# Optimization experiments

Measured on AMD Instinct MI355X. Metric: run time of the kernel, lower is better.

## Reference

```python
import jax, jax.numpy as jnp
import numpy as np

CK, CV, CS = 8, 120, 64          # key / value / spatial-basis channels
NUM_AGENTS, NQ_PER = 4, 4        # queries chunked per agent; chunk(a,4) hard-codes NQ_PER=4
HID = 256                        # lstm_hidden_size
NA = 18                          # num_actions
U = 8                            # Fourier freqs; CS = U*U = 64
MLP_W = 512                      # q/a mlp hidden width


def spatial_basis(h, w):
    # fixed (h, w, CS) cos-product Fourier basis (SpatialBasis buffer)
    ph = jnp.arange(1, h + 1, dtype=jnp.float32)[:, None] * jnp.ones((1, w), jnp.float32) * (np.pi / h)
    pw = jnp.ones((h, 1), jnp.float32) * jnp.arange(1, w + 1, dtype=jnp.float32)[None, :] * (np.pi / w)
    u = jnp.arange(1, U + 1, dtype=jnp.float32)
    ca = jnp.cos(ph[..., None] * u)   # (h, w, U)
    cb = jnp.cos(pw[..., None] * u)   # (h, w, U)
    return jnp.einsum('hwu,hwv->hwuv', ca, cb).reshape(h, w, U * U)


def mlp3(x, w0, b0, w1, b1, w2, b2):
    # build_mlp with 2 relu hidden layers + identity output
    x = jax.nn.relu(x @ w0 + b0)
    x = jax.nn.relu(x @ w1 + b1)
    return x @ w2 + b2


def lstm_cell(x, h, c, w_ih, w_hh, b_ih, b_hh):
    gates = x @ w_ih.T + b_ih + h @ w_hh.T + b_hh
    i, f, g, o = jnp.split(gates, 4, axis=1)
    c2 = jax.nn.sigmoid(f) * c + jax.nn.sigmoid(i) * jnp.tanh(g)
    return jax.nn.sigmoid(o) * jnp.tanh(c2), c2


def setup_inputs() -> dict:
    key = jax.random.key(0)
    ks = jax.random.split(key, 24)
    n, h, w = 128, 64, 64
    s = 0.02
    nq = NUM_AGENTS * NQ_PER
    q_out = nq * (CK + CS)                       # 1152
    a_in = NQ_PER * (CK + 2 * CS + CV) + 2       # 1026
    r = lambda k, shp: jax.random.normal(k, shp, jnp.float32)
    return {
        'x': r(ks[0], (n, h, w, CK + CV)),
        'c': 1,
        'r_prev': r(ks[1], (n,)),
        'a_prev': r(ks[2], (n,)),
        'prev_hidden': r(ks[3], (n, HID)),
        'prev_cell': r(ks[4], (n, HID)),
        'q_w0': r(ks[5], (HID, MLP_W)) * s, 'q_b0': jnp.zeros((MLP_W,), jnp.float32),
        'q_w1': r(ks[6], (MLP_W, MLP_W)) * s, 'q_b1': jnp.zeros((MLP_W,), jnp.float32),
        'q_w2': r(ks[7], (MLP_W, q_out)) * s, 'q_b2': jnp.zeros((q_out,), jnp.float32),
        'a_w0': r(ks[8], (a_in, MLP_W)) * s, 'a_b0': jnp.zeros((MLP_W,), jnp.float32),
        'a_w1': r(ks[9], (MLP_W, MLP_W)) * s, 'a_b1': jnp.zeros((MLP_W,), jnp.float32),
        'a_w2': r(ks[10], (MLP_W, HID)) * s, 'a_b2': jnp.zeros((HID,), jnp.float32),
        'w_ih': r(ks[11], (4 * HID, HID)) * s, 'w_hh': r(ks[12], (4 * HID, HID)) * s,
        'b_ih': jnp.zeros((4 * HID,), jnp.float32), 'b_hh': jnp.zeros((4 * HID,), jnp.float32),
        'p_w': r(ks[13], (HID, NA)) * s, 'p_b': jnp.zeros((NA,), jnp.float32),
        'v_w': r(ks[14], (HID, NA)) * s, 'v_b': jnp.zeros((NA,), jnp.float32),
    }


def reference(x, c, r_prev, a_prev, prev_hidden, prev_cell,
              q_w0, q_b0, q_w1, q_b1, q_w2, q_b2,
              a_w0, a_b0, a_w1, a_b1, a_w2, a_b2,
              w_ih, w_hh, b_ih, b_hh, p_w, p_b, v_w, v_b):
    n, h, w, _ = x.shape
    S = spatial_basis(h, w)
    Sb = jnp.broadcast_to(S, (n, h, w, CS))
    K = jnp.concatenate([x[..., :CK], Sb], axis=-1)   # (n,h,w,CK+CS)
    V = jnp.concatenate([x[..., CK:], Sb], axis=-1)   # (n,h,w,CV+CS)
    # queries from previous hidden state, take agent c's chunk
    Q = mlp3(prev_hidden, q_w0, q_b0, q_w1, q_b1, q_w2, q_b2)
    Q = Q.reshape(n, NUM_AGENTS * NQ_PER, CK + CS)[:, c * NQ_PER:(c + 1) * NQ_PER, :]  # (n,4,CK+CS)
    # spatial QK attention with softmax over the h*w grid
    A = jnp.einsum('nhwd,nqd->nhwq', K, Q)            # (n,h,w,4)
    A = jax.nn.softmax(A.reshape(n, h * w, NQ_PER), axis=1).reshape(n, h, w, NQ_PER)
    a = jnp.einsum('nhwq,nhwd->nqd', A, V)            # (n,4,CV+CS)
    # concat answers + queries + prev reward/action scalars
    answer = jnp.concatenate([a.reshape(n, -1), Q.reshape(n, -1),
                              r_prev[:, None], a_prev[:, None]], axis=1)  # (n,1026)
    answer = mlp3(answer, a_w0, a_b0, a_w1, a_b1, a_w2, a_b2)             # (n,HID)
    hN, _cN = lstm_cell(answer, prev_hidden, prev_cell, w_ih, w_hh, b_ih, b_hh)
    logits = hN @ p_w + p_b
    values = hN @ v_w + v_b
    return logits, values
```

## Files before the change

kernel.cpp:

```cpp
#include <hip/hip_runtime.h>
#include <math.h>

#define NTOT   128
#define NPOS   4096
#define PVCH   8
#define PVLEN  512

__global__ __launch_bounds__(256) void k_gemm(
    const float* __restrict__ Ad, const float* __restrict__ pA,
    const float* __restrict__ biasA, int nzA, int reluA,
    const float* __restrict__ pvR,
    const float* __restrict__ W, float* __restrict__ pbuf,
    int N, int K, int ldw, int gkc, const int* __restrict__ cptr, int cmul) {
  __shared__ float Xs[4][128];
  const int t  = threadIdx.x;
  const int j  = blockIdx.x * 256 + t;
  const int m0 = blockIdx.y * 4;
  const int k0 = blockIdx.z * gkc;
  const int klen = min(gkc, K - k0);
  const int coff = cptr[0] * cmul;

  for (int idx = t; idx < 4 * klen; idx += 256) {
    int mi = idx / klen;
    int kk = idx - mi * klen;
    int col = k0 + kk;
    float s;
    if (Ad) {
      bool pv = false;
      int q = 0, d = 0;
      if (pvR && col < 736) {
        q = col / 184; d = col - q * 184;
        pv = (d < 120);
      }
      if (pv) {
        const size_t eo = (size_t)(m0 + mi) * 480 + q * 120 + d;
        float s0 = pvR[(size_t)(0 * NTOT) * 480 + eo];
        float s1 = pvR[(size_t)(1 * NTOT) * 480 + eo];
        float s2 = pvR[(size_t)(2 * NTOT) * 480 + eo];
        float s3 = pvR[(size_t)(3 * NTOT) * 480 + eo];
        s0 += pvR[(size_t)(4 * NTOT) * 480 + eo];
        s1 += pvR[(size_t)(5 * NTOT) * 480 + eo];
        s2 += pvR[(size_t)(6 * NTOT) * 480 + eo];
        s3 += pvR[(size_t)(7 * NTOT) * 480 + eo];
        s = (s0 + s1) + (s2 + s3);
      } else {
        s = Ad[(size_t)(m0 + mi) * K + col];
      }
    } else {
      float s0 = biasA[col], s1 = 0.f, s2 = 0.f, s3 = 0.f;
      int z = 0;
      for (; z + 4 <= nzA; z += 4) {
        s0 += pA[((size_t)(z + 0) * NTOT + m0 + mi) * K + col];
        s1 += pA[((size_t)(z + 1) * NTOT + m0 + mi) * K + col];
        s2 += pA[((size_t)(z + 2) * NTOT + m0 + mi) * K + col];
        s3 += pA[((size_t)(z + 3) * NTOT + m0 + mi) * K + col];
      }
      for (; z < nzA; ++z) s0 += pA[((size_t)z * NTOT + m0 + mi) * K + col];
      s = (s0 + s1) + (s2 + s3);
      if (reluA) s = fmaxf(s, 0.f);
    }
    Xs[mi][kk] = s;
  }
  __syncthreads();

  if (j < N) {
    float acc[4];
#pragma unroll
    for (int mi = 0; mi < 4; ++mi) acc[mi] = 0.f;
    const float* wp = W + (size_t)k0 * ldw + coff + j;
#pragma unroll 16
    for (int kk = 0; kk < klen; ++kk) {
      float wv = wp[(size_t)kk * ldw];
#pragma unroll
      for (int mi = 0; mi < 4; ++mi) acc[mi] = fmaf(Xs[mi][kk], wv, acc[mi]);
    }
    float* op = pbuf + ((size_t)blockIdx.z * NTOT + m0) * N + j;
#pragma unroll
    for (int mi = 0; mi < 4; ++mi) op[(size_t)mi * N] = acc[mi];
  }
}

__global__ __launch_bounds__(1024) void k_logits(
    const float* __restrict__ x, const float* __restrict__ pQ,
    const float* __restrict__ q_b2, const int* __restrict__ cptr,
    const float* __restrict__ r_prev, const float* __restrict__ a_prev,
    float* __restrict__ Pw, float* __restrict__ ans) {
  const int n = blockIdx.x;
  const int t = threadIdx.x;
  const int wave = t >> 6, lane = t & 63;

  __shared__ float Qs[4][72];
  __shared__ float ct[64][8];
  __shared__ float cbQ[4 * 576];
  __shared__ float4 wlds[NPOS];
  __shared__ float red[4][16];
  __shared__ float mfin[4], lfin[4];
  __shared__ float rowSum[64][4][8];

  const float PI64 = 3.14159265358979323846f / 64.f;

  if (t < 288) {
    const int coff = cptr[0] * 288;
    float s = q_b2[coff + t];
#pragma unroll
    for (int z = 0; z < 8; ++z) s += pQ[((size_t)z * NTOT + n) * 288 + t];
    Qs[t / 72][t % 72] = s;
  }
  if (t < 512) {
    int i = t >> 3, u = t & 7;
    ct[i][u] = cosf((float)((i + 1) * (u + 1)) * PI64);
  }
  __syncthreads();

  for (int e = t; e < 2048; e += 1024) {
    int q = e >> 9, j = (e >> 3) & 63, u = e & 7;
    float s = 0.f;
#pragma unroll
    for (int v = 0; v < 8; ++v) s += ct[j][v] * Qs[q][8 + u * 8 + v];
    cbQ[q * 576 + j * 9 + u] = s;
  }
  __syncthreads();

  const float* xp = x + (size_t)n * NPOS * 128;
  float lmax[4] = {-1e30f, -1e30f, -1e30f, -1e30f};
#pragma unroll
  for (int r = 0; r < 4; ++r) {
    const int pos = r * 1024 + t;
    const int i = r * 16 + wave;
    const float4* xr = reinterpret_cast<const float4*>(xp + (size_t)pos * 128);
    float4 xa = xr[0], xb = xr[1];
    float lg[4];
#pragma unroll
    for (int q = 0; q < 4; ++q) {
      float s = xa.x * Qs[q][0] + xa.y * Qs[q][1] + xa.z * Qs[q][2] + xa.w * Qs[q][3]
              + xb.x * Qs[q][4] + xb.y * Qs[q][5] + xb.z * Qs[q][6] + xb.w * Qs[q][7];
      const float* cq = cbQ + q * 576 + lane * 9;
      float s2 = 0.f;
#pragma unroll
      for (int u = 0; u < 8; ++u) s2 += ct[i][u] * cq[u];
      lg[q] = s + s2;
      lmax[q] = fmaxf(lmax[q], lg[q]);
    }
    wlds[pos] = make_float4(lg[0], lg[1], lg[2], lg[3]);
  }

#pragma unroll
  for (int off = 32; off; off >>= 1)
#pragma unroll
    for (int q = 0; q < 4; ++q) lmax[q] = fmaxf(lmax[q], __shfl_xor(lmax[q], off));
  if (lane == 0)
#pragma unroll
    for (int q = 0; q < 4; ++q) red[q][wave] = lmax[q];
  __syncthreads();
  if (t < 4) {
    float m = red[t][0];
#pragma unroll
    for (int w = 1; w < 16; ++w) m = fmaxf(m, red[t][w]);
    mfin[t] = m;
  }
  __syncthreads();

  float lsum[4] = {0.f, 0.f, 0.f, 0.f};
#pragma unroll
  for (int r = 0; r < 4; ++r) {
    const int pos = r * 1024 + t;
    float4 w = wlds[pos];
    w.x = __expf(w.x - mfin[0]);
    w.y = __expf(w.y - mfin[1]);
    w.z = __expf(w.z - mfin[2]);
    w.w = __expf(w.w - mfin[3]);
    wlds[pos] = w;
    lsum[0] += w.x; lsum[1] += w.y; lsum[2] += w.z; lsum[3] += w.w;
  }
#pragma unroll
  for (int off = 32; off; off >>= 1)
#pragma unroll
    for (int q = 0; q < 4; ++q) lsum[q] += __shfl_xor(lsum[q], off);
  if (lane == 0)
#pragma unroll
    for (int q = 0; q < 4; ++q) red[q][wave] = lsum[q];
  __syncthreads();
  if (t < 4) {
    float s = 0.f;
#pragma unroll
    for (int w = 0; w < 16; ++w) s += red[t][w];
    lfin[t] = s;
  }
  __syncthreads();

  const float i0 = 1.f / lfin[0], i1 = 1.f / lfin[1];
  const float i2 = 1.f / lfin[2], i3 = 1.f / lfin[3];

  float4* Pw4 = reinterpret_cast<float4*>(Pw) + (size_t)n * NPOS;
#pragma unroll
  for (int r = 0; r < 4; ++r) {
    const int pos = r * 1024 + t;
    float4 w = wlds[pos];
    Pw4[pos] = make_float4(w.x * i0, w.y * i1, w.z * i2, w.w * i3);
  }

  for (int o = t; o < 2048; o += 1024) {
    int i = o >> 5, q = (o >> 3) & 3, v = o & 7;
    float s0 = 0.f, s1 = 0.f, s2 = 0.f, s3 = 0.f;
    const float* wb = reinterpret_cast<const float*>(&wlds[i * 64]) + q;
#pragma unroll 8
    for (int j = 0; j < 64; j += 4) {
      s0 += wb[(j + 0) * 4] * ct[j + 0][v];
      s1 += wb[(j + 1) * 4] * ct[j + 1][v];
      s2 += wb[(j + 2) * 4] * ct[j + 2][v];
      s3 += wb[(j + 3) * 4] * ct[j + 3][v];
    }
    float inv = (q == 0) ? i0 : (q == 1) ? i1 : (q == 2) ? i2 : i3;
    rowSum[i][q][v] = ((s0 + s1) + (s2 + s3)) * inv;
  }
  __syncthreads();

  float* ap = ans + (size_t)n * 1026;
  if (t < 256) {
    int q = t >> 6, uv = t & 63, u = uv >> 3, v = uv & 7;
    float s = 0.f;
#pragma unroll 8
    for (int i = 0; i < 64; ++i) s += ct[i][u] * rowSum[i][q][v];
    ap[q * 184 + 120 + uv] = s;
  } else if (t < 544) {
    int qi = t - 256;
    ap[736 + qi] = Qs[qi / 72][qi % 72];
  } else if (t == 544) {
    ap[1024] = r_prev[n];
  } else if (t == 545) {
    ap[1025] = a_prev[n];
  }
}

__global__ __launch_bounds__(256, 4) void k_pv(
    const float* __restrict__ x, const float* __restrict__ Pw,
    float* __restrict__ pvp) {
  const int n = blockIdx.y, ck = blockIdx.x;
  const int t = threadIdx.x, wave = t >> 6, lane = t & 63;
  __shared__ float4 wl[PVLEN];
  __shared__ __align__(16) float part[4][4][120];

  const int base = ck * PVLEN;
  {
    const float4* src = reinterpret_cast<const float4*>(Pw) + (size_t)n * NPOS + base;
    wl[t] = src[t];
    wl[t + 256] = src[t + 256];
  }
  __syncthreads();

  const int xl = (lane < 60) ? lane : 59;
  const float* vb = x + ((size_t)n * NPOS + base + wave * 128) * 128 + 8 + 2 * xl;

  float ax0[4] = {0.f, 0.f, 0.f, 0.f};
  float ax1[4] = {0.f, 0.f, 0.f, 0.f};
#pragma unroll
  for (int b = 0; b < 8; ++b) {
    float2 v0  = *reinterpret_cast<const float2*>(vb + (size_t)(b * 16 + 0)  * 128);
    float2 v1  = *reinterpret_cast<const float2*>(vb + (size_t)(b * 16 + 1)  * 128);
    float2 v2  = *reinterpret_cast<const float2*>(vb + (size_t)(b * 16 + 2)  * 128);
    float2 v3  = *reinterpret_cast<const float2*>(vb + (size_t)(b * 16 + 3)  * 128);
    float2 v4  = *reinterpret_cast<const float2*>(vb + (size_t)(b * 16 + 4)  * 128);
    float2 v5  = *reinterpret_cast<const float2*>(vb + (size_t)(b * 16 + 5)  * 128);
    float2 v6  = *reinterpret_cast<const float2*>(vb + (size_t)(b * 16 + 6)  * 128);
    float2 v7  = *reinterpret_cast<const float2*>(vb + (size_t)(b * 16 + 7)  * 128);
    float2 v8  = *reinterpret_cast<const float2*>(vb + (size_t)(b * 16 + 8)  * 128);
    float2 v9  = *reinterpret_cast<const float2*>(vb + (size_t)(b * 16 + 9)  * 128);
    float2 v10 = *reinterpret_cast<const float2*>(vb + (size_t)(b * 16 + 10) * 128);
    float2 v11 = *reinterpret_cast<const float2*>(vb + (size_t)(b * 16 + 11) * 128);
    float2 v12 = *reinterpret_cast<const float2*>(vb + (size_t)(b * 16 + 12) * 128);
    float2 v13 = *reinterpret_cast<const float2*>(vb + (size_t)(b * 16 + 13) * 128);
    float2 v14 = *reinterpret_cast<const float2*>(vb + (size_t)(b * 16 + 14) * 128);
    float2 v15 = *reinterpret_cast<const float2*>(vb + (size_t)(b * 16 + 15) * 128);
#define ACC(VV, II)                                                              \
    {                                                                            \
      float4 w = wl[wave * 128 + b * 16 + II];                                   \
      ax0[0] += w.x * VV.x; ax1[0] += w.x * VV.y;                                \
      ax0[1] += w.y * VV.x; ax1[1] += w.y * VV.y;                                \
      ax0[2] += w.z * VV.x; ax1[2] += w.z * VV.y;                                \
      ax0[3] += w.w * VV.x; ax1[3] += w.w * VV.y;                                \
    }
    ACC(v0, 0)  ACC(v1, 1)  ACC(v2, 2)  ACC(v3, 3)
    ACC(v4, 4)  ACC(v5, 5)  ACC(v6, 6)  ACC(v7, 7)
    ACC(v8, 8)  ACC(v9, 9)  ACC(v10, 10) ACC(v11, 11)
    ACC(v12, 12) ACC(v13, 13) ACC(v14, 14) ACC(v15, 15)
#undef ACC
  }
  if (lane < 60) {
#pragma unroll
    for (int q = 0; q < 4; ++q)
      *reinterpret_cast<float2*>(&part[wave][q][2 * lane]) = make_float2(ax0[q], ax1[q]);
  }
  __syncthreads();

  float* op = pvp + ((size_t)ck * NTOT + n) * 480;
  for (int idx = t; idx < 480; idx += 256) {
    const int q = idx / 120, d = idx - q * 120;
    op[idx] = (part[0][q][d] + part[1][q][d]) + (part[2][q][d] + part[3][q][d]);
  }
}

__global__ __launch_bounds__(256) void k_gates(
    const float* __restrict__ pA, const float* __restrict__ biasA,
    const float* __restrict__ hp,
    const float* __restrict__ w_ih, const float* __restrict__ w_hh,
    const float* __restrict__ b_ih, const float* __restrict__ b_hh,
    float* __restrict__ gbuf) {
  const int t = threadIdx.x;
  const int n0 = blockIdx.x * 2;
  const int r0 = blockIdx.y * 64;
  __shared__ float xs[2][256], hs[2][256];
  __shared__ float red[64][4][5];
#pragma unroll
  for (int s = 0; s < 2; ++s) {
    float v0 = biasA[t], v1 = 0.f, v2 = 0.f, v3 = 0.f;
#pragma unroll
    for (int z = 0; z < 8; z += 4) {
      v0 += pA[((size_t)(z + 0) * NTOT + n0 + s) * 256 + t];
      v1 += pA[((size_t)(z + 1) * NTOT + n0 + s) * 256 + t];
      v2 += pA[((size_t)(z + 2) * NTOT + n0 + s) * 256 + t];
      v3 += pA[((size_t)(z + 3) * NTOT + n0 + s) * 256 + t];
    }
    xs[s][t] = (v0 + v1) + (v2 + v3);
    hs[s][t] = hp[(size_t)(n0 + s) * 256 + t];
  }
  __syncthreads();
  const int r = t >> 2, kq = t & 3;
  const int row = r0 + r;
  const float4* wi = reinterpret_cast<const float4*>(w_ih + (size_t)row * 256 + kq * 64);
  const float4* wh = reinterpret_cast<const float4*>(w_hh + (size_t)row * 256 + kq * 64);
  float s00 = 0.f, s01 = 0.f, s10 = 0.f, s11 = 0.f;
#pragma unroll
  for (int i = 0; i < 16; ++i) {
    float4 a = wi[i], b = wh[i];
    const int k4 = kq * 64 + i * 4;
    s00 += a.x * xs[0][k4] + a.y * xs[0][k4 + 1] + a.z * xs[0][k4 + 2] + a.w * xs[0][k4 + 3];
    s01 += a.x * xs[1][k4] + a.y * xs[1][k4 + 1] + a.z * xs[1][k4 + 2] + a.w * xs[1][k4 + 3];
    s10 += b.x * hs[0][k4] + b.y * hs[0][k4 + 1] + b.z * hs[0][k4 + 2] + b.w * hs[0][k4 + 3];
    s11 += b.x * hs[1][k4] + b.y * hs[1][k4 + 1] + b.z * hs[1][k4 + 2] + b.w * hs[1][k4 + 3];
  }
  red[r][kq][0] = s00; red[r][kq][1] = s01; red[r][kq][2] = s10; red[r][kq][3] = s11;
  __syncthreads();
  if (t < 128) {
    const int rr = t >> 1, s = t & 1;
    float g = b_ih[r0 + rr] + b_hh[r0 + rr];
#pragma unroll
    for (int k = 0; k < 4; ++k) g += red[rr][k][s] + red[rr][k][2 + s];
    gbuf[(size_t)(n0 + s) * 1024 + r0 + rr] = g;
  }
}

__global__ __launch_bounds__(256) void k_lstm2(
    const float* __restrict__ gbuf, const float* __restrict__ cp,
    const float* __restrict__ p_w, const float* __restrict__ p_b,
    const float* __restrict__ v_w, const float* __restrict__ v_b,
    float* __restrict__ out) {
  const int t = threadIdx.x;
  const int n0 = blockIdx.x * 2;
  __shared__ float h2[2][256];
#pragma unroll
  for (int s = 0; s < 2; ++s) {
    const size_t gb = (size_t)(n0 + s) * 1024;
    float gi = gbuf[gb + t], gf = gbuf[gb + 256 + t];
    float gg = gbuf[gb + 512 + t], go = gbuf[gb + 768 + t];
    float si = 1.f / (1.f + __expf(-gi));
    float sf = 1.f / (1.f + __expf(-gf));
    float so = 1.f / (1.f + __expf(-go));
    float c2 = sf * cp[(size_t)(n0 + s) * 256 + t] + si * tanhf(gg);
    h2[s][t] = so * tanhf(c2);
  }
  __syncthreads();
  if (t < 72) {
    const int si = t / 36, r = t % 36, iv = r / 18, j = r % 18;
    const float* W = iv ? v_w : p_w;
    const float* B = iv ? v_b : p_b;
    float s = B[j];
#pragma unroll 8
    for (int k = 0; k < 256; ++k) s += h2[si][k] * W[k * 18 + j];
    out[(size_t)iv * (NTOT * 18) + (size_t)(n0 + si) * 18 + j] = s;
  }
}

extern "C" void kernel_launch(void* const* d_in, const int* in_sizes, int n_in,
                              void* d_out, int out_size, void* d_ws, size_t ws_size,
                              hipStream_t stream) {
  const float* x      = (const float*)d_in[0];
  const int*   cptr   = (const int*)d_in[1];
  const float* r_prev = (const float*)d_in[2];
  const float* a_prev = (const float*)d_in[3];
  const float* hprev  = (const float*)d_in[4];
  const float* cprev  = (const float*)d_in[5];
  const float* q_w0 = (const float*)d_in[6];
  const float* q_b0 = (const float*)d_in[7];
  const float* q_w1 = (const float*)d_in[8];
  const float* q_b1 = (const float*)d_in[9];
  const float* q_w2 = (const float*)d_in[10];
  const float* q_b2 = (const float*)d_in[11];
  const float* a_w0 = (const float*)d_in[12];
  const float* a_b0 = (const float*)d_in[13];
  const float* a_w1 = (const float*)d_in[14];
  const float* a_b1 = (const float*)d_in[15];
  const float* a_w2 = (const float*)d_in[16];
  const float* a_b2 = (const float*)d_in[17];
  const float* w_ih = (const float*)d_in[18];
  const float* w_hh = (const float*)d_in[19];
  const float* b_ih = (const float*)d_in[20];
  const float* b_hh = (const float*)d_in[21];
  const float* p_w  = (const float*)d_in[22];
  const float* p_b  = (const float*)d_in[23];
  const float* v_w  = (const float*)d_in[24];
  const float* v_b  = (const float*)d_in[25];
  float* out = (float*)d_out;
  float* ws  = (float*)d_ws;

  float* pQ  = ws;
  float* pb1 = pQ  + 294912;
  float* pb2 = pb1 + 589824;
  float* pb3 = pb2 + 524288;
  float* Pw  = pb3 + 262144;
  float* pvp = Pw  + 2097152;
  float* ans = pvp + 491520;
  float* gbuf= ans + 131328;

  k_gemm<<<dim3(2, 32, 4), 256, 0, stream>>>(hprev, nullptr, nullptr, 0, 0, nullptr,
                                             q_w0, pb1, 512, 256, 512, 64, cptr, 0);
  k_gemm<<<dim3(2, 32, 8), 256, 0, stream>>>(nullptr, pb1, q_b0, 4, 1, nullptr,
                                             q_w1, pb2, 512, 512, 512, 64, cptr, 0);
  k_gemm<<<dim3(2, 32, 8), 256, 0, stream>>>(nullptr, pb2, q_b1, 8, 1, nullptr,
                                             q_w2, pQ, 288, 512, 1152, 64, cptr, 288);

  k_logits<<<NTOT, 1024, 0, stream>>>(x, pQ, q_b2, cptr, r_prev, a_prev, Pw, ans);
  k_pv<<<dim3(PVCH, NTOT), 256, 0, stream>>>(x, Pw, pvp);

  k_gemm<<<dim3(2, 32, 9), 256, 0, stream>>>(ans, nullptr, nullptr, 0, 0, pvp,
                                             a_w0, pb1, 512, 1026, 512, 128, cptr, 0);
  k_gemm<<<dim3(2, 32, 8), 256, 0, stream>>>(nullptr, pb1, a_b0, 9, 1, nullptr,
                                             a_w1, pb2, 512, 512, 512, 64, cptr, 0);
  k_gemm<<<dim3(1, 32, 8), 256, 0, stream>>>(nullptr, pb2, a_b1, 8, 1, nullptr,
                                             a_w2, pb3, 256, 512, 256, 64, cptr, 0);

  k_gates<<<dim3(64, 16), 256, 0, stream>>>(pb3, a_b2, hprev, w_ih, w_hh, b_ih, b_hh, gbuf);
  k_lstm2<<<64, 256, 0, stream>>>(gbuf, cprev, p_w, p_b, v_w, v_b, out);
}
```

Baseline: 139.8 us.

## Fuse each three-layer MLP into one kernel with activations kept in shared memory

Replaces the six split-K GEMM launches (three per MLP) with two fused kernels, k_mlpq and k_mlpa. Each runs one 1024-thread block per 4 rows and keeps hidden activations in LDS, so partial-sum buffers and their cross-kernel reductions are gone. This cuts launch count and global round-trips. In exchange only 32 blocks run, far fewer than before, so each block streams the full weight matrices and parallelism over the GPU's CUs drops sharply, which may leave the weight loads bandwidth-starved.

```diff
diff --git a/kernel.cpp b/kernel.cpp
--- a/kernel.cpp
+++ b/kernel.cpp
@@ -6,83 +6,101 @@
 #define PVCH   8
 #define PVLEN  512
 
-__global__ __launch_bounds__(256) void k_gemm(
-    const float* __restrict__ Ad, const float* __restrict__ pA,
-    const float* __restrict__ biasA, int nzA, int reluA,
-    const float* __restrict__ pvR,
-    const float* __restrict__ W, float* __restrict__ pbuf,
-    int N, int K, int ldw, int gkc, const int* __restrict__ cptr, int cmul) {
-  __shared__ float Xs[4][128];
-  const int t  = threadIdx.x;
-  const int j  = blockIdx.x * 256 + t;
-  const int m0 = blockIdx.y * 4;
-  const int k0 = blockIdx.z * gkc;
-  const int klen = min(gkc, K - k0);
-  const int coff = cptr[0] * cmul;
-
-  for (int idx = t; idx < 4 * klen; idx += 256) {
-    int mi = idx / klen;
-    int kk = idx - mi * klen;
-    int col = k0 + kk;
-    float s;
-    if (Ad) {
-      bool pv = false;
-      int q = 0, d = 0;
-      if (pvR && col < 736) {
-        q = col / 184; d = col - q * 184;
-        pv = (d < 120);
+__global__ __launch_bounds__(1024) void k_mlpq(
+    const float* __restrict__ hp,
+    const float* __restrict__ q_w0, const float* __restrict__ q_b0,
+    const float* __restrict__ q_w1, const float* __restrict__ q_b1,
+    const float* __restrict__ q_w2, const float* __restrict__ q_b2,
+    const int* __restrict__ cptr, float* __restrict__ Qb) {
+  const int t = threadIdx.x;
+  const int m0 = blockIdx.x * 4;
+  __shared__ float xs[4][256];
+  __shared__ float h1[4][512];
+  __shared__ float h2[4][512];
+  __shared__ float tmp[4][512];
+
+  {
+    int mi = t >> 8, k = t & 255;
+    xs[mi][k] = hp[(size_t)(m0 + mi) * 256 + k];
+  }
+  __syncthreads();
+
+  {
+    const int j = t & 511, kh = t >> 9;
+    const float* wp = q_w0 + (size_t)(kh * 128) * 512 + j;
+    float a0 = 0.f, a1 = 0.f, a2 = 0.f, a3 = 0.f;
+#pragma unroll 8
+    for (int k = 0; k < 128; ++k) {
+      float wv = wp[(size_t)k * 512];
+      int kk = kh * 128 + k;
+      a0 += wv * xs[0][kk]; a1 += wv * xs[1][kk];
+      a2 += wv * xs[2][kk]; a3 += wv * xs[3][kk];
+    }
+    if (kh == 0) { tmp[0][j] = a0; tmp[1][j] = a1; tmp[2][j] = a2; tmp[3][j] = a3; }
+    __syncthreads();
+    if (kh == 1) {
+      float b = q_b0[j];
+      h1[0][j] = fmaxf(tmp[0][j] + a0 + b, 0.f);
+      h1[1][j] = fmaxf(tmp[1][j] + a1 + b, 0.f);
+      h1[2][j] = fmaxf(tmp[2][j] + a2 + b, 0.f);
+      h1[3][j] = fmaxf(tmp[3][j] + a3 + b, 0.f);
+    }
+    __syncthreads();
+  }
+
+  {
+    const int j = t & 511, kh = t >> 9;
+    const float* wp = q_w1 + (size_t)(kh * 256) * 512 + j;
+    float a0 = 0.f, a1 = 0.f, a2 = 0.f, a3 = 0.f;
+#pragma unroll 8
+    for (int k = 0; k < 256; ++k) {
+      float wv = wp[(size_t)k * 512];
+      int kk = kh * 256 + k;
+      a0 += wv * h1[0][kk]; a1 += wv * h1[1][kk];
+      a2 += wv * h1[2][kk]; a3 += wv * h1[3][kk];
+    }
+    if (kh == 0) { tmp[0][j] = a0; tmp[1][j] = a1; tmp[2][j] = a2; tmp[3][j] = a3; }
+    __syncthreads();
+    if (kh == 1) {
+      float b = q_b1[j];
+      h2[0][j] = fmaxf(tmp[0][j] + a0 + b, 0.f);
+      h2[1][j] = fmaxf(tmp[1][j] + a1 + b, 0.f);
+      h2[2][j] = fmaxf(tmp[2][j] + a2 + b, 0.f);
+      h2[3][j] = fmaxf(tmp[3][j] + a3 + b, 0.f);
+    }
+    __syncthreads();
+  }
+
+  {
+    const int coff = cptr[0] * 288;
+    const bool act = t < 576;
+    const int j = (t < 288) ? t : t - 288;
+    const int kh = (t < 288) ? 0 : 1;
+    float a0 = 0.f, a1 = 0.f, a2 = 0.f, a3 = 0.f;
+    if (act) {
+      const float* wp = q_w2 + (size_t)(kh * 256) * 1152 + coff + j;
+#pragma unroll 8
+      for (int k = 0; k < 256; ++k) {
+        float wv = wp[(size_t)k * 1152];
+        int kk = kh * 256 + k;
+        a0 += wv * h2[0][kk]; a1 += wv * h2[1][kk];
+        a2 += wv * h2[2][kk]; a3 += wv * h2[3][kk];
       }
-      if (pv) {
-        const size_t eo = (size_t)(m0 + mi) * 480 + q * 120 + d;
-        float s0 = pvR[(size_t)(0 * NTOT) * 480 + eo];
-        float s1 = pvR[(size_t)(1 * NTOT) * 480 + eo];
-        float s2 = pvR[(size_t)(2 * NTOT) * 480 + eo];
-        float s3 = pvR[(size_t)(3 * NTOT) * 480 + eo];
-        s0 += pvR[(size_t)(4 * NTOT) * 480 + eo];
-        s1 += pvR[(size_t)(5 * NTOT) * 480 + eo];
-        s2 += pvR[(size_t)(6 * NTOT) * 480 + eo];
-        s3 += pvR[(size_t)(7 * NTOT) * 480 + eo];
-        s = (s0 + s1) + (s2 + s3);
-      } else {
-        s = Ad[(size_t)(m0 + mi) * K + col];
-      }
-    } else {
-      float s0 = biasA[col], s1 = 0.f, s2 = 0.f, s3 = 0.f;
-      int z = 0;
-      for (; z + 4 <= nzA; z += 4) {
-        s0 += pA[((size_t)(z + 0) * NTOT + m0 + mi) * K + col];
-        s1 += pA[((size_t)(z + 1) * NTOT + m0 + mi) * K + col];
-        s2 += pA[((size_t)(z + 2) * NTOT + m0 + mi) * K + col];
-        s3 += pA[((size_t)(z + 3) * NTOT + m0 + mi) * K + col];
-      }
-      for (; z < nzA; ++z) s0 += pA[((size_t)z * NTOT + m0 + mi) * K + col];
-      s = (s0 + s1) + (s2 + s3);
-      if (reluA) s = fmaxf(s, 0.f);
-    }
-    Xs[mi][kk] = s;
-  }
-  __syncthreads();
-
-  if (j < N) {
-    float acc[4];
-#pragma unroll
-    for (int mi = 0; mi < 4; ++mi) acc[mi] = 0.f;
-    const float* wp = W + (size_t)k0 * ldw + coff + j;
-#pragma unroll 16
-    for (int kk = 0; kk < klen; ++kk) {
-      float wv = wp[(size_t)kk * ldw];
-#pragma unroll
-      for (int mi = 0; mi < 4; ++mi) acc[mi] = fmaf(Xs[mi][kk], wv, acc[mi]);
-    }
-    float* op = pbuf + ((size_t)blockIdx.z * NTOT + m0) * N + j;
-#pragma unroll
-    for (int mi = 0; mi < 4; ++mi) op[(size_t)mi * N] = acc[mi];
+      if (kh == 0) { tmp[0][j] = a0; tmp[1][j] = a1; tmp[2][j] = a2; tmp[3][j] = a3; }
+    }
+    __syncthreads();
+    if (act && kh == 1) {
+      float b = q_b2[coff + j];
+      Qb[(size_t)(m0 + 0) * 288 + j] = tmp[0][j] + a0 + b;
+      Qb[(size_t)(m0 + 1) * 288 + j] = tmp[1][j] + a1 + b;
+      Qb[(size_t)(m0 + 2) * 288 + j] = tmp[2][j] + a2 + b;
+      Qb[(size_t)(m0 + 3) * 288 + j] = tmp[3][j] + a3 + b;
+    }
   }
 }
 
 __global__ __launch_bounds__(1024) void k_logits(
-    const float* __restrict__ x, const float* __restrict__ pQ,
-    const float* __restrict__ q_b2, const int* __restrict__ cptr,
+    const float* __restrict__ x, const float* __restrict__ Qb,
     const float* __restrict__ r_prev, const float* __restrict__ a_prev,
     float* __restrict__ Pw, float* __restrict__ ans) {
   const int n = blockIdx.x;
@@ -99,13 +117,7 @@
 
   const float PI64 = 3.14159265358979323846f / 64.f;
 
-  if (t < 288) {
-    const int coff = cptr[0] * 288;
-    float s = q_b2[coff + t];
-#pragma unroll
-    for (int z = 0; z < 8; ++z) s += pQ[((size_t)z * NTOT + n) * 288 + t];
-    Qs[t / 72][t % 72] = s;
-  }
+  if (t < 288) Qs[t / 72][t % 72] = Qb[(size_t)n * 288 + t];
   if (t < 512) {
     int i = t >> 3, u = t & 7;
     ct[i][u] = cosf((float)((i + 1) * (u + 1)) * PI64);
@@ -299,9 +311,114 @@
   }
 }
 
+__global__ __launch_bounds__(1024) void k_mlpa(
+    const float* __restrict__ ans, const float* __restrict__ pvp,
+    const float* __restrict__ a_w0, const float* __restrict__ a_b0,
+    const float* __restrict__ a_w1, const float* __restrict__ a_b1,
+    const float* __restrict__ a_w2, const float* __restrict__ a_b2,
+    float* __restrict__ am) {
+  const int t = threadIdx.x;
+  const int m0 = blockIdx.x * 4;
+  __shared__ float xs[4][1032];
+  __shared__ float h1[4][512];
+  __shared__ float h2[4][512];
+  __shared__ float tmp[4][512];
+
+  for (int idx = t; idx < 4 * 1026; idx += 1024) {
+    int mi = idx / 1026, col = idx - mi * 1026;
+    float s;
+    int q = col / 184, d = col - q * 184;
+    if (col < 736 && d < 120) {
+      const size_t eo = (size_t)(m0 + mi) * 480 + q * 120 + d;
+      float s0 = pvp[(size_t)(0 * NTOT) * 480 + eo];
+      float s1 = pvp[(size_t)(1 * NTOT) * 480 + eo];
+      float s2 = pvp[(size_t)(2 * NTOT) * 480 + eo];
+      float s3 = pvp[(size_t)(3 * NTOT) * 480 + eo];
+      s0 += pvp[(size_t)(4 * NTOT) * 480 + eo];
+      s1 += pvp[(size_t)(5 * NTOT) * 480 + eo];
+      s2 += pvp[(size_t)(6 * NTOT) * 480 + eo];
+      s3 += pvp[(size_t)(7 * NTOT) * 480 + eo];
+      s = (s0 + s1) + (s2 + s3);
+    } else {
+      s = ans[(size_t)(m0 + mi) * 1026 + col];
+    }
+    xs[mi][col] = s;
+  }
+  __syncthreads();
+
+  {
+    const int j = t & 511, kh = t >> 9;
+    const float* wp = a_w0 + (size_t)(kh * 513) * 512 + j;
+    float a0 = 0.f, a1 = 0.f, a2 = 0.f, a3 = 0.f;
+#pragma unroll 8
+    for (int k = 0; k < 513; ++k) {
+      float wv = wp[(size_t)k * 512];
+      int kk = kh * 513 + k;
+      a0 += wv * xs[0][kk]; a1 += wv * xs[1][kk];
+      a2 += wv * xs[2][kk]; a3 += wv * xs[3][kk];
+    }
+    if (kh == 0) { tmp[0][j] = a0; tmp[1][j] = a1; tmp[2][j] = a2; tmp[3][j] = a3; }
+    __syncthreads();
+    if (kh == 1) {
+      float b = a_b0[j];
+      h1[0][j] = fmaxf(tmp[0][j] + a0 + b, 0.f);
+      h1[1][j] = fmaxf(tmp[1][j] + a1 + b, 0.f);
+      h1[2][j] = fmaxf(tmp[2][j] + a2 + b, 0.f);
+      h1[3][j] = fmaxf(tmp[3][j] + a3 + b, 0.f);
+    }
+    __syncthreads();
+  }
+
+  {
+    const int j = t & 511, kh = t >> 9;
+    const float* wp = a_w1 + (size_t)(kh * 256) * 512 + j;
+    float a0 = 0.f, a1 = 0.f, a2 = 0.f, a3 = 0.f;
+#pragma unroll 8
+    for (int k = 0; k < 256; ++k) {
+      float wv = wp[(size_t)k * 512];
+      int kk = kh * 256 + k;
+      a0 += wv * h1[0][kk]; a1 += wv * h1[1][kk];
+      a2 += wv * h1[2][kk]; a3 += wv * h1[3][kk];
+    }
+    if (kh == 0) { tmp[0][j] = a0; tmp[1][j] = a1; tmp[2][j] = a2; tmp[3][j] = a3; }
+    __syncthreads();
+    if (kh == 1) {
+      float b = a_b1[j];
+      h2[0][j] = fmaxf(tmp[0][j] + a0 + b, 0.f);
+      h2[1][j] = fmaxf(tmp[1][j] + a1 + b, 0.f);
+      h2[2][j] = fmaxf(tmp[2][j] + a2 + b, 0.f);
+      h2[3][j] = fmaxf(tmp[3][j] + a3 + b, 0.f);
+    }
+    __syncthreads();
+  }
+
+  {
+    const int j = t & 255, kq = t >> 8;
+    const float* wp = a_w2 + (size_t)(kq * 128) * 256 + j;
+    float a0 = 0.f, a1 = 0.f, a2 = 0.f, a3 = 0.f;
+#pragma unroll 8
+    for (int k = 0; k < 128; ++k) {
+      float wv = wp[(size_t)k * 256];
+      int kk = kq * 128 + k;
+      a0 += wv * h2[0][kk]; a1 += wv * h2[1][kk];
+      a2 += wv * h2[2][kk]; a3 += wv * h2[3][kk];
+    }
+    if (kq == 0) { tmp[0][j] = a0; tmp[1][j] = a1; tmp[2][j] = a2; tmp[3][j] = a3; }
+    if (kq == 1) { tmp[0][256 + j] = a0; tmp[1][256 + j] = a1; tmp[2][256 + j] = a2; tmp[3][256 + j] = a3; }
+    if (kq == 2) { h1[0][j] = a0; h1[1][j] = a1; h1[2][j] = a2; h1[3][j] = a3; }
+    __syncthreads();
+    if (kq == 3) {
+      float b = a_b2[j];
+      am[(size_t)(m0 + 0) * 256 + j] = tmp[0][j] + tmp[0][256 + j] + h1[0][j] + a0 + b;
+      am[(size_t)(m0 + 1) * 256 + j] = tmp[1][j] + tmp[1][256 + j] + h1[1][j] + a1 + b;
+      am[(size_t)(m0 + 2) * 256 + j] = tmp[2][j] + tmp[2][256 + j] + h1[2][j] + a2 + b;
+      am[(size_t)(m0 + 3) * 256 + j] = tmp[3][j] + tmp[3][256 + j] + h1[3][j] + a3 + b;
+    }
+  }
+}
+
 __global__ __launch_bounds__(256) void k_gates(
-    const float* __restrict__ pA, const float* __restrict__ biasA,
-    const float* __restrict__ hp,
+    const float* __restrict__ am, const float* __restrict__ hp,
     const float* __restrict__ w_ih, const float* __restrict__ w_hh,
     const float* __restrict__ b_ih, const float* __restrict__ b_hh,
     float* __restrict__ gbuf) {
@@ -312,15 +429,7 @@
   __shared__ float red[64][4][5];
 #pragma unroll
   for (int s = 0; s < 2; ++s) {
-    float v0 = biasA[t], v1 = 0.f, v2 = 0.f, v3 = 0.f;
-#pragma unroll
-    for (int z = 0; z < 8; z += 4) {
-      v0 += pA[((size_t)(z + 0) * NTOT + n0 + s) * 256 + t];
-      v1 += pA[((size_t)(z + 1) * NTOT + n0 + s) * 256 + t];
-      v2 += pA[((size_t)(z + 2) * NTOT + n0 + s) * 256 + t];
-      v3 += pA[((size_t)(z + 3) * NTOT + n0 + s) * 256 + t];
-    }
-    xs[s][t] = (v0 + v1) + (v2 + v3);
+    xs[s][t] = am[(size_t)(n0 + s) * 256 + t];
     hs[s][t] = hp[(size_t)(n0 + s) * 256 + t];
   }
   __syncthreads();
@@ -412,32 +521,20 @@
   float* out = (float*)d_out;
   float* ws  = (float*)d_ws;
 
-  float* pQ  = ws;
-  float* pb1 = pQ  + 294912;
-  float* pb2 = pb1 + 589824;
-  float* pb3 = pb2 + 524288;
-  float* Pw  = pb3 + 262144;
+  float* Qb  = ws;
+  float* Pw  = Qb  + 36864;
   float* pvp = Pw  + 2097152;
   float* ans = pvp + 491520;
-  float* gbuf= ans + 131328;
-
-  k_gemm<<<dim3(2, 32, 4), 256, 0, stream>>>(hprev, nullptr, nullptr, 0, 0, nullptr,
-                                             q_w0, pb1, 512, 256, 512, 64, cptr, 0);
-  k_gemm<<<dim3(2, 32, 8), 256, 0, stream>>>(nullptr, pb1, q_b0, 4, 1, nullptr,
-                                             q_w1, pb2, 512, 512, 512, 64, cptr, 0);
-  k_gemm<<<dim3(2, 32, 8), 256, 0, stream>>>(nullptr, pb2, q_b1, 8, 1, nullptr,
-                                             q_w2, pQ, 288, 512, 1152, 64, cptr, 288);
-
-  k_logits<<<NTOT, 1024, 0, stream>>>(x, pQ, q_b2, cptr, r_prev, a_prev, Pw, ans);
+  float* am  = ans + 131328;
+  float* gbuf= am  + 32768;
+
+  k_mlpq<<<32, 1024, 0, stream>>>(hprev, q_w0, q_b0, q_w1, q_b1, q_w2, q_b2, cptr, Qb);
+
+  k_logits<<<NTOT, 1024, 0, stream>>>(x, Qb, r_prev, a_prev, Pw, ans);
   k_pv<<<dim3(PVCH, NTOT), 256, 0, stream>>>(x, Pw, pvp);
 
-  k_gemm<<<dim3(2, 32, 9), 256, 0, stream>>>(ans, nullptr, nullptr, 0, 0, pvp,
-                                             a_w0, pb1, 512, 1026, 512, 128, cptr, 0);
-  k_gemm<<<dim3(2, 32, 8), 256, 0, stream>>>(nullptr, pb1, a_b0, 9, 1, nullptr,
-                                             a_w1, pb2, 512, 512, 512, 64, cptr, 0);
-  k_gemm<<<dim3(1, 32, 8), 256, 0, stream>>>(nullptr, pb2, a_b1, 8, 1, nullptr,
-                                             a_w2, pb3, 256, 512, 256, 64, cptr, 0);
-
-  k_gates<<<dim3(64, 16), 256, 0, stream>>>(pb3, a_b2, hprev, w_ih, w_hh, b_ih, b_hh, gbuf);
+  k_mlpa<<<32, 1024, 0, stream>>>(ans, pvp, a_w0, a_b0, a_w1, a_b1, a_w2, a_b2, am);
+
+  k_gates<<<dim3(64, 16), 256, 0, stream>>>(am, hprev, w_ih, w_hh, b_ih, b_hh, gbuf);
   k_lstm2<<<64, 256, 0, stream>>>(gbuf, cprev, p_w, p_b, v_w, v_b, out);
 }
```

New measurement: 212.7 us. 52.2% more time.

## Split spatial softmax into per-chunk partials with flash-style rescaling

Applied to the files above, without the earlier changes.

The logits/softmax kernel, formerly one 1024-thread block per sample, becomes 4 chunk blocks per sample. Each block computes local max and sum, writes unnormalized exp weights and per-chunk row partials, and stores its stats. A new finalize kernel combines the stats into per-chunk scales and finishes the spatial-basis answer. The PV partials are rescaled by those scales when loaded in the first answer GEMM. This raises parallelism and cuts per-block LDS, in exchange for an extra kernel launch and more global traffic for the partials.

```diff
diff --git a/kernel.cpp b/kernel.cpp
--- a/kernel.cpp
+++ b/kernel.cpp
@@ -5,11 +5,13 @@
 #define NPOS   4096
 #define PVCH   8
 #define PVLEN  512
+#define LCH    4
+#define LCLEN  1024
 
 __global__ __launch_bounds__(256) void k_gemm(
     const float* __restrict__ Ad, const float* __restrict__ pA,
     const float* __restrict__ biasA, int nzA, int reluA,
-    const float* __restrict__ pvR,
+    const float* __restrict__ pvR, const float* __restrict__ scl,
     const float* __restrict__ W, float* __restrict__ pbuf,
     int N, int K, int ldw, int gkc, const int* __restrict__ cptr, int cmul) {
   __shared__ float Xs[4][128];
@@ -34,15 +36,17 @@
       }
       if (pv) {
         const size_t eo = (size_t)(m0 + mi) * 480 + q * 120 + d;
-        float s0 = pvR[(size_t)(0 * NTOT) * 480 + eo];
-        float s1 = pvR[(size_t)(1 * NTOT) * 480 + eo];
-        float s2 = pvR[(size_t)(2 * NTOT) * 480 + eo];
-        float s3 = pvR[(size_t)(3 * NTOT) * 480 + eo];
-        s0 += pvR[(size_t)(4 * NTOT) * 480 + eo];
-        s1 += pvR[(size_t)(5 * NTOT) * 480 + eo];
-        s2 += pvR[(size_t)(6 * NTOT) * 480 + eo];
-        s3 += pvR[(size_t)(7 * NTOT) * 480 + eo];
-        s = (s0 + s1) + (s2 + s3);
+        const float* scp = scl + (size_t)(m0 + mi) * 16 + q;
+        float p0 = pvR[(size_t)(0 * NTOT) * 480 + eo];
+        float p1 = pvR[(size_t)(1 * NTOT) * 480 + eo];
+        float p2 = pvR[(size_t)(2 * NTOT) * 480 + eo];
+        float p3 = pvR[(size_t)(3 * NTOT) * 480 + eo];
+        float p4 = pvR[(size_t)(4 * NTOT) * 480 + eo];
+        float p5 = pvR[(size_t)(5 * NTOT) * 480 + eo];
+        float p6 = pvR[(size_t)(6 * NTOT) * 480 + eo];
+        float p7 = pvR[(size_t)(7 * NTOT) * 480 + eo];
+        s = scp[0] * (p0 + p1) + scp[4] * (p2 + p3)
+          + scp[8] * (p4 + p5) + scp[12] * (p6 + p7);
       } else {
         s = Ad[(size_t)(m0 + mi) * K + col];
       }
@@ -80,39 +84,42 @@
   }
 }
 
-__global__ __launch_bounds__(1024) void k_logits(
+__global__ __launch_bounds__(256) void k_logit_part(
     const float* __restrict__ x, const float* __restrict__ pQ,
     const float* __restrict__ q_b2, const int* __restrict__ cptr,
     const float* __restrict__ r_prev, const float* __restrict__ a_prev,
-    float* __restrict__ Pw, float* __restrict__ ans) {
-  const int n = blockIdx.x;
-  const int t = threadIdx.x;
+    float* __restrict__ Pw, float* __restrict__ stats,
+    float* __restrict__ rowSumP, float* __restrict__ ans) {
+  const int ck = blockIdx.x;
+  const int n  = blockIdx.y;
+  const int t  = threadIdx.x;
   const int wave = t >> 6, lane = t & 63;
 
   __shared__ float Qs[4][72];
   __shared__ float ct[64][8];
   __shared__ float cbQ[4 * 576];
-  __shared__ float4 wlds[NPOS];
-  __shared__ float red[4][16];
+  __shared__ float4 wlds[LCLEN];
+  __shared__ float red[4][4];
   __shared__ float mfin[4], lfin[4];
-  __shared__ float rowSum[64][4][8];
 
   const float PI64 = 3.14159265358979323846f / 64.f;
 
-  if (t < 288) {
+  {
     const int coff = cptr[0] * 288;
-    float s = q_b2[coff + t];
-#pragma unroll
-    for (int z = 0; z < 8; ++z) s += pQ[((size_t)z * NTOT + n) * 288 + t];
-    Qs[t / 72][t % 72] = s;
-  }
-  if (t < 512) {
-    int i = t >> 3, u = t & 7;
+    for (int idx = t; idx < 288; idx += 256) {
+      float s = q_b2[coff + idx];
+#pragma unroll
+      for (int z = 0; z < 8; ++z) s += pQ[((size_t)z * NTOT + n) * 288 + idx];
+      Qs[idx / 72][idx % 72] = s;
+    }
+  }
+  for (int e = t; e < 512; e += 256) {
+    int i = e >> 3, u = e & 7;
     ct[i][u] = cosf((float)((i + 1) * (u + 1)) * PI64);
   }
   __syncthreads();
 
-  for (int e = t; e < 2048; e += 1024) {
+  for (int e = t; e < 2048; e += 256) {
     int q = e >> 9, j = (e >> 3) & 63, u = e & 7;
     float s = 0.f;
 #pragma unroll
@@ -121,12 +128,15 @@
   }
   __syncthreads();
 
+  const int base = ck * LCLEN;
   const float* xp = x + (size_t)n * NPOS * 128;
+
   float lmax[4] = {-1e30f, -1e30f, -1e30f, -1e30f};
 #pragma unroll
   for (int r = 0; r < 4; ++r) {
-    const int pos = r * 1024 + t;
-    const int i = r * 16 + wave;
+    const int local = r * 256 + t;
+    const int pos = base + local;
+    const int i = ck * 16 + r * 4 + wave;
     const float4* xr = reinterpret_cast<const float4*>(xp + (size_t)pos * 128);
     float4 xa = xr[0], xb = xr[1];
     float lg[4];
@@ -141,7 +151,7 @@
       lg[q] = s + s2;
       lmax[q] = fmaxf(lmax[q], lg[q]);
     }
-    wlds[pos] = make_float4(lg[0], lg[1], lg[2], lg[3]);
+    wlds[local] = make_float4(lg[0], lg[1], lg[2], lg[3]);
   }
 
 #pragma unroll
@@ -152,24 +162,21 @@
 #pragma unroll
     for (int q = 0; q < 4; ++q) red[q][wave] = lmax[q];
   __syncthreads();
-  if (t < 4) {
-    float m = red[t][0];
-#pragma unroll
-    for (int w = 1; w < 16; ++w) m = fmaxf(m, red[t][w]);
-    mfin[t] = m;
-  }
-  __syncthreads();
-
+  if (t < 4) mfin[t] = fmaxf(fmaxf(red[t][0], red[t][1]), fmaxf(red[t][2], red[t][3]));
+  __syncthreads();
+
+  float4* Pw4 = reinterpret_cast<float4*>(Pw) + (size_t)n * NPOS + base;
   float lsum[4] = {0.f, 0.f, 0.f, 0.f};
 #pragma unroll
   for (int r = 0; r < 4; ++r) {
-    const int pos = r * 1024 + t;
-    float4 w = wlds[pos];
+    const int local = r * 256 + t;
+    float4 w = wlds[local];
     w.x = __expf(w.x - mfin[0]);
     w.y = __expf(w.y - mfin[1]);
     w.z = __expf(w.z - mfin[2]);
     w.w = __expf(w.w - mfin[3]);
-    wlds[pos] = w;
+    wlds[local] = w;
+    Pw4[local] = w;
     lsum[0] += w.x; lsum[1] += w.y; lsum[2] += w.z; lsum[3] += w.w;
   }
 #pragma unroll
@@ -181,28 +188,16 @@
     for (int q = 0; q < 4; ++q) red[q][wave] = lsum[q];
   __syncthreads();
   if (t < 4) {
-    float s = 0.f;
-#pragma unroll
-    for (int w = 0; w < 16; ++w) s += red[t][w];
-    lfin[t] = s;
-  }
-  __syncthreads();
-
-  const float i0 = 1.f / lfin[0], i1 = 1.f / lfin[1];
-  const float i2 = 1.f / lfin[2], i3 = 1.f / lfin[3];
-
-  float4* Pw4 = reinterpret_cast<float4*>(Pw) + (size_t)n * NPOS;
-#pragma unroll
-  for (int r = 0; r < 4; ++r) {
-    const int pos = r * 1024 + t;
-    float4 w = wlds[pos];
-    Pw4[pos] = make_float4(w.x * i0, w.y * i1, w.z * i2, w.w * i3);
-  }
-
-  for (int o = t; o < 2048; o += 1024) {
+    lfin[t] = red[t][0] + red[t][1] + red[t][2] + red[t][3];
+    stats[((size_t)n * LCH + ck) * 8 + t] = mfin[t];
+    stats[((size_t)n * LCH + ck) * 8 + 4 + t] = lfin[t];
+  }
+  __syncthreads();
+
+  for (int o = t; o < 512; o += 256) {
     int i = o >> 5, q = (o >> 3) & 3, v = o & 7;
+    const float* wb = reinterpret_cast<const float*>(&wlds[i * 64]) + q;
     float s0 = 0.f, s1 = 0.f, s2 = 0.f, s3 = 0.f;
-    const float* wb = reinterpret_cast<const float*>(&wlds[i * 64]) + q;
 #pragma unroll 8
     for (int j = 0; j < 64; j += 4) {
       s0 += wb[(j + 0) * 4] * ct[j + 0][v];
@@ -210,25 +205,56 @@
       s2 += wb[(j + 2) * 4] * ct[j + 2][v];
       s3 += wb[(j + 3) * 4] * ct[j + 3][v];
     }
-    float inv = (q == 0) ? i0 : (q == 1) ? i1 : (q == 2) ? i2 : i3;
-    rowSum[i][q][v] = ((s0 + s1) + (s2 + s3)) * inv;
-  }
-  __syncthreads();
-
-  float* ap = ans + (size_t)n * 1026;
-  if (t < 256) {
-    int q = t >> 6, uv = t & 63, u = uv >> 3, v = uv & 7;
+    rowSumP[(((size_t)n * LCH + ck) * 16 + i) * 32 + q * 8 + v] = (s0 + s1) + (s2 + s3);
+  }
+
+  if (ck == 0) {
+    float* ap = ans + (size_t)n * 1026;
+    for (int idx = t; idx < 288; idx += 256) ap[736 + idx] = Qs[idx / 72][idx % 72];
+    if (t == 0) { ap[1024] = r_prev[n]; ap[1025] = a_prev[n]; }
+  }
+}
+
+__global__ __launch_bounds__(256) void k_fin(
+    const float* __restrict__ stats, const float* __restrict__ rowSumP,
+    float* __restrict__ scales, float* __restrict__ ans) {
+  const int n = blockIdx.x, t = threadIdx.x;
+  __shared__ float ct[64][8];
+  __shared__ float sc[LCH][4];
+  const float PI64 = 3.14159265358979323846f / 64.f;
+
+  for (int e = t; e < 512; e += 256) {
+    int i = e >> 3, u = e & 7;
+    ct[i][u] = cosf((float)((i + 1) * (u + 1)) * PI64);
+  }
+  if (t < 16) {
+    const int q = t & 3, ck = t >> 2;
+    float M = -1e30f;
+#pragma unroll
+    for (int c = 0; c < LCH; ++c) M = fmaxf(M, stats[((size_t)n * LCH + c) * 8 + q]);
+    float L = 0.f;
+#pragma unroll
+    for (int c = 0; c < LCH; ++c)
+      L += stats[((size_t)n * LCH + c) * 8 + 4 + q] *
+           __expf(stats[((size_t)n * LCH + c) * 8 + q] - M);
+    sc[ck][q] = __expf(stats[((size_t)n * LCH + ck) * 8 + q] - M) / L;
+  }
+  __syncthreads();
+  if (t < 16) scales[(size_t)n * 16 + t] = sc[t >> 2][t & 3];
+
+  {
+    const int q = t >> 6, uv = t & 63, u = uv >> 3, v = uv & 7;
     float s = 0.f;
-#pragma unroll 8
-    for (int i = 0; i < 64; ++i) s += ct[i][u] * rowSum[i][q][v];
-    ap[q * 184 + 120 + uv] = s;
-  } else if (t < 544) {
-    int qi = t - 256;
-    ap[736 + qi] = Qs[qi / 72][qi % 72];
-  } else if (t == 544) {
-    ap[1024] = r_prev[n];
-  } else if (t == 545) {
-    ap[1025] = a_prev[n];
+#pragma unroll
+    for (int ck = 0; ck < LCH; ++ck) {
+      float ss = 0.f;
+#pragma unroll 4
+      for (int i = 0; i < 16; ++i)
+        ss += ct[ck * 16 + i][u] *
+              rowSumP[(((size_t)n * LCH + ck) * 16 + i) * 32 + q * 8 + v];
+      s += sc[ck][q] * ss;
+    }
+    ans[(size_t)n * 1026 + q * 184 + 120 + uv] = s;
   }
 }
 
@@ -412,30 +438,35 @@
   float* out = (float*)d_out;
   float* ws  = (float*)d_ws;
 
-  float* pQ  = ws;
-  float* pb1 = pQ  + 294912;
-  float* pb2 = pb1 + 589824;
-  float* pb3 = pb2 + 524288;
-  float* Pw  = pb3 + 262144;
-  float* pvp = Pw  + 2097152;
-  float* ans = pvp + 491520;
-  float* gbuf= ans + 131328;
-
-  k_gemm<<<dim3(2, 32, 4), 256, 0, stream>>>(hprev, nullptr, nullptr, 0, 0, nullptr,
+  float* pQ   = ws;
+  float* pb1  = pQ   + 294912;
+  float* pb2  = pb1  + 589824;
+  float* pb3  = pb2  + 524288;
+  float* Pw   = pb3  + 262144;
+  float* pvp  = Pw   + 2097152;
+  float* ans  = pvp  + 491520;
+  float* gbuf = ans  + 131328;
+  float* stats= gbuf + 131072;
+  float* rsum = stats+ 4096;
+  float* scl  = rsum + 262144;
+
+  k_gemm<<<dim3(2, 32, 4), 256, 0, stream>>>(hprev, nullptr, nullptr, 0, 0, nullptr, nullptr,
                                              q_w0, pb1, 512, 256, 512, 64, cptr, 0);
-  k_gemm<<<dim3(2, 32, 8), 256, 0, stream>>>(nullptr, pb1, q_b0, 4, 1, nullptr,
+  k_gemm<<<dim3(2, 32, 8), 256, 0, stream>>>(nullptr, pb1, q_b0, 4, 1, nullptr, nullptr,
                                              q_w1, pb2, 512, 512, 512, 64, cptr, 0);
-  k_gemm<<<dim3(2, 32, 8), 256, 0, stream>>>(nullptr, pb2, q_b1, 8, 1, nullptr,
+  k_gemm<<<dim3(2, 32, 8), 256, 0, stream>>>(nullptr, pb2, q_b1, 8, 1, nullptr, nullptr,
                                              q_w2, pQ, 288, 512, 1152, 64, cptr, 288);
 
-  k_logits<<<NTOT, 1024, 0, stream>>>(x, pQ, q_b2, cptr, r_prev, a_prev, Pw, ans);
+  k_logit_part<<<dim3(LCH, NTOT), 256, 0, stream>>>(x, pQ, q_b2, cptr, r_prev, a_prev,
+                                                    Pw, stats, rsum, ans);
   k_pv<<<dim3(PVCH, NTOT), 256, 0, stream>>>(x, Pw, pvp);
-
-  k_gemm<<<dim3(2, 32, 9), 256, 0, stream>>>(ans, nullptr, nullptr, 0, 0, pvp,
+  k_fin<<<NTOT, 256, 0, stream>>>(stats, rsum, scl, ans);
+
+  k_gemm<<<dim3(2, 32, 9), 256, 0, stream>>>(ans, nullptr, nullptr, 0, 0, pvp, scl,
                                              a_w0, pb1, 512, 1026, 512, 128, cptr, 0);
-  k_gemm<<<dim3(2, 32, 8), 256, 0, stream>>>(nullptr, pb1, a_b0, 9, 1, nullptr,
+  k_gemm<<<dim3(2, 32, 8), 256, 0, stream>>>(nullptr, pb1, a_b0, 9, 1, nullptr, nullptr,
                                              a_w1, pb2, 512, 512, 512, 64, cptr, 0);
-  k_gemm<<<dim3(1, 32, 8), 256, 0, stream>>>(nullptr, pb2, a_b1, 8, 1, nullptr,
+  k_gemm<<<dim3(1, 32, 8), 256, 0, stream>>>(nullptr, pb2, a_b1, 8, 1, nullptr, nullptr,
                                              a_w2, pb3, 256, 512, 256, 64, cptr, 0);
 
   k_gates<<<dim3(64, 16), 256, 0, stream>>>(pb3, a_b2, hprev, w_ih, w_hh, b_ih, b_hh, gbuf);
```

Result: slower. 143.4 us (+2.6%).
